# Performance work log

Measured on AMD Instinct MI355X. Metric: run time of the kernel, lower is better.

The kernel has to match this reference:

```python
import jax, jax.numpy as jnp
import numpy as np


def setup_inputs() -> dict:
    key = jax.random.key(0)
    ks = jax.random.split(key, 8)
    B, N, K, C_in, M, C_add, C_out = 2, 40000, 16, 64, 16, 3, 128
    in_features = (C_in + C_add) * M  # 1072
    input_features = jax.random.normal(ks[0], (B, N, C_in), dtype=jnp.float32)
    neighbor_inds = jax.random.randint(ks[1], (B, N, K), 0, N, dtype=jnp.int64)
    inverse_neighbors = jax.random.randint(ks[2], (B, N * K), 0, N * K, dtype=jnp.int64)
    inverse_k = jax.random.randint(ks[3], (B, N * K), 0, K, dtype=jnp.int64)
    inverse_idx = jax.random.randint(ks[4], (B, N * K), 0, N, dtype=jnp.int64)
    weightnet = jax.random.normal(ks[5], (B, N, K, M), dtype=jnp.float32)
    additional_features = jax.random.normal(ks[6], (B, N, K, C_add), dtype=jnp.float32)
    bound = 1.0 / np.sqrt(in_features)
    kw, kb = jax.random.split(ks[7])
    linear_weight = jax.random.uniform(kw, (C_out, in_features), dtype=jnp.float32, minval=-bound, maxval=bound)
    linear_bias = jax.random.uniform(kb, (C_out,), dtype=jnp.float32, minval=-bound, maxval=bound)
    return {
        "input_features": input_features,
        "neighbor_inds": neighbor_inds,
        "inverse_neighbors": inverse_neighbors,
        "inverse_k": inverse_k,
        "inverse_idx": inverse_idx,
        "weightnet": weightnet,
        "additional_features": additional_features,
        "linear_weight": linear_weight,
        "linear_bias": linear_bias,
    }


def reference(input_features, neighbor_inds, inverse_neighbors, inverse_k, inverse_idx,
              weightnet, additional_features, linear_weight, linear_bias):
    # inverse_* tensors are only used by the custom CUDA backward; unused here.
    B, N, K = neighbor_inds.shape
    # gather neighbor features: [B, N, K, C_in]
    gathered = jnp.take_along_axis(input_features[:, :, None, :],
                                   neighbor_inds[..., None], axis=1)
    # concat extra per-neighbor features -> [B, N, K, C]
    feats = jnp.concatenate([gathered, additional_features], axis=-1)
    # PConv: [B,N,C,K] @ [B,N,K,M] -> [B,N,C,M] -> flatten to [B,N,C*M]
    pconv = jnp.einsum('bnkc,bnkm->bncm', feats, weightnet)
    pconv = pconv.reshape(B, N, -1)
    # fused linear
    out = jnp.einsum('bnf,of->bno', pconv, linear_weight) + linear_bias
    return out
```

## Files before the change

### kernel.cpp

```cpp
#include <hip/hip_runtime.h>
#include <stdint.h>

typedef unsigned short u16;
typedef short short8 __attribute__((ext_vector_type(8)));
typedef float floatx4 __attribute__((ext_vector_type(4)));

#define NPERB   40000
#define NPTS    80000
#define KNBR    16
#define CIN     64
#define MDIM    16
#define CADD    3
#define CF      (CIN + CADD)
#define COUT    128
#define KF      1072
#define KP      1088
#define NKT     34
#define PTSB    16
#define SLAB    65
#define GR      128
#define PPB     8

__device__ __forceinline__ u16 f2bf(float f) {
    union { float f; unsigned int u; } v; v.f = f;
    unsigned int u = v.u;
    return (u16)((u + 0x7FFFu + ((u >> 16) & 1u)) >> 16);
}
__device__ __forceinline__ short8 pack8(floatx4 x, floatx4 y) {
    union { short8 v; u16 a[8]; } u;
    u.a[0] = f2bf(x[0]); u.a[1] = f2bf(x[1]); u.a[2] = f2bf(x[2]); u.a[3] = f2bf(x[3]);
    u.a[4] = f2bf(y[0]); u.a[5] = f2bf(y[1]); u.a[6] = f2bf(y[2]); u.a[7] = f2bf(y[3]);
    return u.v;
}
__device__ __forceinline__ unsigned swz(unsigned chunk) {
    return chunk ^ ((chunk >> 3) & 7u);
}
__device__ __forceinline__ void gload_lds16(const void* g, void* l) {
    __builtin_amdgcn_global_load_lds(
        (const __attribute__((address_space(1))) void*)g,
        (__attribute__((address_space(3))) void*)l, 16, 0, 0);
}

__global__ void prep_lw_kernel(const float* __restrict__ lw, u16* __restrict__ lwp) {
    int i = blockIdx.x * 256 + threadIdx.x;
    if (i >= COUT * KP) return;
    int o = i / KP, f = i - o * KP;
    lwp[i] = (f < KF) ? f2bf(lw[(size_t)o * KF + f]) : (u16)0;
}

__device__ __forceinline__ void emit_point(
    int lane, float av, const float (&fv)[KNBR], const float* wl,
    u16* __restrict__ dst)
{
    const int em = lane & 15, ec = lane >> 4;
    float ev = 0.f;
#pragma unroll
    for (int k = 0; k < KNBR; k++)
        ev += __shfl(av, k * CADD + ec) * wl[k * MDIM + em];
    if (ec == 3) ev = 0.f;
    dst[1024 + lane] = f2bf(ev);

    floatx4 a0 = 0, a1 = 0, a2 = 0, a3 = 0;
#pragma unroll
    for (int k = 0; k < KNBR; k++) {
        const floatx4* w4 = (const floatx4*)(wl + k * MDIM);
        const float fvk = fv[k];
        a0 += fvk * w4[0]; a1 += fvk * w4[1];
        a2 += fvk * w4[2]; a3 += fvk * w4[3];
    }
    *(short8*)(dst + lane * 16)     = pack8(a0, a1);
    *(short8*)(dst + lane * 16 + 8) = pack8(a2, a3);
}

__global__ __launch_bounds__(256) void pconv_kernel(
    const float* __restrict__ inp,
    const int*   __restrict__ nbr,
    const float* __restrict__ wn,
    const float* __restrict__ addl,
    u16* __restrict__ pc)
{
    __shared__ __align__(16) float Wns[PPB * KNBR * MDIM];

    const int wave = threadIdx.x >> 6;
    const int lane = threadIdx.x & 63;
    const int pbase = blockIdx.x * PPB;
    const float* inpb = inp + ((pbase >= NPERB) ? (size_t)NPERB * CIN : 0);

    const int pr0 = wave * 2;
    const int p0  = __builtin_amdgcn_readfirstlane(pbase + pr0);
    const int p1  = p0 + 1;

    float* wl0 = Wns + pr0 * (KNBR * MDIM);
    float* wl1 = wl0 + KNBR * MDIM;
    gload_lds16(wn + (size_t)p0 * (KNBR * MDIM) + lane * 4, wl0);
    gload_lds16(wn + (size_t)p1 * (KNBR * MDIM) + lane * 4, wl1);

    float av0 = (lane < KNBR * CADD) ? addl[(size_t)p0 * (KNBR * CADD) + lane] : 0.f;
    float av1 = (lane < KNBR * CADD) ? addl[(size_t)p1 * (KNBR * CADD) + lane] : 0.f;

    const int* nb0 = nbr + (size_t)p0 * KNBR;
    const int* nb1 = nbr + (size_t)p1 * KNBR;
    int idx0[KNBR], idx1[KNBR];
#pragma unroll
    for (int k = 0; k < KNBR; k++) idx0[k] = nb0[k];
#pragma unroll
    for (int k = 0; k < KNBR; k++) idx1[k] = nb1[k];

    float fv0[KNBR], fv1[KNBR];
#pragma unroll
    for (int k = 0; k < KNBR; k++) fv0[k] = inpb[(size_t)idx0[k] * CIN + lane];
#pragma unroll
    for (int k = 0; k < KNBR; k++) fv1[k] = inpb[(size_t)idx1[k] * CIN + lane];

    asm volatile("s_waitcnt vmcnt(0)" ::: "memory");
    __builtin_amdgcn_sched_barrier(0);

    emit_point(lane, av0, fv0, wl0, pc + (size_t)p0 * KP);
    emit_point(lane, av1, fv1, wl1, pc + (size_t)p1 * KP);
}

__global__ __launch_bounds__(256, 2) void gemm_kernel(
    const u16* __restrict__ pc,
    const u16* __restrict__ lwp,
    const float* __restrict__ bias,
    float* __restrict__ out)
{
    __shared__ __align__(16) u16 As[4][4][1024];

    const int wave = threadIdx.x >> 6;
    const int lane = threadIdx.x & 63;
    const int r16 = lane & 15, quad = lane >> 4;
    const int row0 = blockIdx.x * GR + wave * 32;

    const u16* aS0 = pc + (size_t)(row0 + r16) * KP + quad * 8;
    const u16* aS1 = aS0 + (size_t)16 * KP;
    u16* aD = &As[wave][0][0];

    const u16* bB = lwp + (size_t)r16 * KP + quad * 8;

    float bv[8];
#pragma unroll
    for (int n = 0; n < 8; n++) bv[n] = bias[n * 16 + r16];
    __builtin_amdgcn_sched_barrier(0);

    floatx4 acc0[8], acc1[8];
#pragma unroll
    for (int n = 0; n < 8; n++) { acc0[n] = 0; acc1[n] = 0; }

    short8 Bq[3][8];

#define STAGE(s) { \
    gload_lds16(aS0 + (s) * 32, aD + ((s) & 3) * 1024); \
    gload_lds16(aS1 + (s) * 32, aD + ((s) & 3) * 1024 + 512); }

#define LOADB(s) { \
    _Pragma("unroll") \
    for (int n = 0; n < 8; n++) \
        Bq[(s) % 3][n] = *(const short8*)(bB + (size_t)n * 16 * KP + (s) * 32); }

    STAGE(0); STAGE(1); STAGE(2);
    __builtin_amdgcn_sched_barrier(0);
    LOADB(0);
    __builtin_amdgcn_sched_barrier(0);
    LOADB(1);
    __builtin_amdgcn_sched_barrier(0);

#define STEP(kt, N) { \
    if ((kt) + 3 < NKT) STAGE((kt) + 3); \
    if ((kt) + 2 < NKT) LOADB((kt) + 2); \
    __builtin_amdgcn_sched_barrier(0); \
    asm volatile("s_waitcnt vmcnt(" #N ")"); \
    __builtin_amdgcn_sched_barrier(0); \
    short8 A0 = *(const short8*)(aD + ((kt) & 3) * 1024 + lane * 8); \
    short8 A1 = *(const short8*)(aD + ((kt) & 3) * 1024 + 512 + lane * 8); \
    asm volatile("s_waitcnt lgkmcnt(0)"); \
    __builtin_amdgcn_sched_barrier(0); \
    _Pragma("unroll") \
    for (int n = 0; n < 8; n++) { \
        acc0[n] = __builtin_amdgcn_mfma_f32_16x16x32_bf16(A0, Bq[(kt) % 3][n], acc0[n], 0, 0, 0); \
        acc1[n] = __builtin_amdgcn_mfma_f32_16x16x32_bf16(A1, Bq[(kt) % 3][n], acc1[n], 0, 0, 0); \
    } }

    STEP(0, 18)  STEP(1, 20)  STEP(2, 20)  STEP(3, 20)  STEP(4, 20)
    STEP(5, 20)  STEP(6, 20)  STEP(7, 20)  STEP(8, 20)  STEP(9, 20)
    STEP(10, 20) STEP(11, 20) STEP(12, 20) STEP(13, 20) STEP(14, 20)
    STEP(15, 20) STEP(16, 20) STEP(17, 20) STEP(18, 20) STEP(19, 20)
    STEP(20, 20) STEP(21, 20) STEP(22, 20) STEP(23, 20) STEP(24, 20)
    STEP(25, 20) STEP(26, 20) STEP(27, 20) STEP(28, 20) STEP(29, 20)
    STEP(30, 20) STEP(31, 18) STEP(32, 8)  STEP(33, 0)

#undef STEP
#undef LOADB
#undef STAGE

#pragma unroll
    for (int n = 0; n < 8; n++) {
#pragma unroll
        for (int r = 0; r < 4; r++) {
            size_t row = (size_t)(row0 + quad * 4 + r) * COUT;
            out[row + n * 16 + r16] = acc0[n][r] + bv[n];
            row = (size_t)(row0 + 16 + quad * 4 + r) * COUT;
            out[row + n * 16 + r16] = acc1[n][r] + bv[n];
        }
    }
}

__device__ __forceinline__ void compute_point(
    int pr, int lane, float av, const float (&fv)[KNBR],
    const float* wl, u16* Apc)
{
    const int em = lane & 15, ec = lane >> 4;
    float ev = 0.f;
#pragma unroll
    for (int k = 0; k < KNBR; k++)
        ev += __shfl(av, k * CADD + ec) * wl[k * MDIM + em];
    if (ec == 3) ev = 0.f;
    {
        unsigned kt   = 32 + (lane >> 5);
        unsigned quad = (lane >> 3) & 3;
        unsigned ch   = kt * SLAB + (unsigned)pr * 4 + quad;
        Apc[swz(ch) * 8 + (lane & 7)] = f2bf(ev);
    }
    floatx4 a0 = 0, a1 = 0, a2 = 0, a3 = 0;
#pragma unroll
    for (int k = 0; k < KNBR; k++) {
        const floatx4* w4 = (const floatx4*)(wl + k * MDIM);
        const float fvk = fv[k];
        a0 += fvk * w4[0]; a1 += fvk * w4[1];
        a2 += fvk * w4[2]; a3 += fvk * w4[3];
    }
    {
        unsigned kt = lane >> 1, qb = (lane & 1) * 2;
        unsigned ch = kt * SLAB + (unsigned)pr * 4 + qb;
        *(short8*)&Apc[swz(ch) * 8]     = pack8(a0, a1);
        *(short8*)&Apc[swz(ch + 1) * 8] = pack8(a2, a3);
    }
}

__global__ __launch_bounds__(512, 6) void fused_kernel(
    const float* __restrict__ inp, const int* __restrict__ nbr,
    const float* __restrict__ wn, const float* __restrict__ addl,
    const u16* __restrict__ lwp, const float* __restrict__ bias,
    float* __restrict__ out)
{
    __shared__ __align__(16) u16   Apc[(NKT * SLAB + 8) * 8];
    __shared__ __align__(16) float Wns[PTSB * KNBR * MDIM];

    const int wave = threadIdx.x >> 6;
    const int lane = threadIdx.x & 63;
    const int pbase = blockIdx.x * PTSB;
    const float* inpb = inp + ((pbase >= NPERB) ? (size_t)NPERB * CIN : 0);

    const int pr0 = wave * 2;
    const int p0  = __builtin_amdgcn_readfirstlane(pbase + pr0);
    const int p1  = p0 + 1;

    float* wl0 = Wns + pr0 * (KNBR * MDIM);
    float* wl1 = wl0 + KNBR * MDIM;
    gload_lds16(wn + (size_t)p0 * (KNBR * MDIM) + lane * 4, wl0);
    gload_lds16(wn + (size_t)p1 * (KNBR * MDIM) + lane * 4, wl1);

    float av0 = (lane < KNBR * CADD) ? addl[(size_t)p0 * (KNBR * CADD) + lane] : 0.f;
    float av1 = (lane < KNBR * CADD) ? addl[(size_t)p1 * (KNBR * CADD) + lane] : 0.f;

    const int* nb0 = nbr + (size_t)p0 * KNBR;
    const int* nb1 = nbr + (size_t)p1 * KNBR;
    int idx0[KNBR], idx1[KNBR];
#pragma unroll
    for (int k = 0; k < KNBR; k++) idx0[k] = nb0[k];
#pragma unroll
    for (int k = 0; k < KNBR; k++) idx1[k] = nb1[k];

    float fv0[KNBR], fv1[KNBR];
#pragma unroll
    for (int k = 0; k < KNBR; k++) fv0[k] = inpb[(size_t)idx0[k] * CIN + lane];
#pragma unroll
    for (int k = 0; k < KNBR; k++) fv1[k] = inpb[(size_t)idx1[k] * CIN + lane];

    asm volatile("s_waitcnt vmcnt(0)" ::: "memory");
    __builtin_amdgcn_sched_barrier(0);

    compute_point(pr0,     lane, av0, fv0, wl0, Apc);
    compute_point(pr0 + 1, lane, av1, fv1, wl1, Apc);

    const int r16 = lane & 15, quad = lane >> 4;
    const int c0 = wave * 16;
    const u16* Bp = lwp + (size_t)(c0 + r16) * KP + quad * 8;
    const unsigned abase = (unsigned)r16 * 4 + quad;
    const float bv = bias[c0 + r16];

    __syncthreads();

    floatx4 acc = 0;
#pragma unroll 2
    for (int kt = 0; kt < NKT; kt++) {
        short8 A = *(const short8*)&Apc[swz((unsigned)kt * SLAB + abase) * 8];
        short8 B = *(const short8*)(Bp + kt * 32);
        acc = __builtin_amdgcn_mfma_f32_16x16x32_bf16(A, B, acc, 0, 0, 0);
    }

#pragma unroll
    for (int r = 0; r < 4; r++) {
        const size_t row = (size_t)(pbase + quad * 4 + r) * COUT;
        out[row + c0 + r16] = acc[r] + bv;
    }
}

__global__ __launch_bounds__(256) void fused_fallback_kernel(
    const float* __restrict__ inp, const int* __restrict__ nbr,
    const float* __restrict__ wn, const float* __restrict__ addl,
    const float* __restrict__ lw, const float* __restrict__ bias,
    float* __restrict__ out)
{
    const int p = blockIdx.x;
    const int b = p / NPERB;
    const int tid = threadIdx.x;
    __shared__ float sf[KNBR * CF];
    __shared__ float sw[KNBR * MDIM];
    __shared__ float sp[KF];

    sw[tid] = wn[(size_t)p * (KNBR * MDIM) + tid];
    for (int i = tid; i < KNBR * CIN; i += 256) {
        int k = i >> 6, c = i & 63;
        int idx = nbr[(size_t)p * KNBR + k];
        sf[k * CF + c] = inp[((size_t)b * NPERB + idx) * CIN + c];
    }
    if (tid < KNBR * CADD) {
        int k = tid / CADD, c = tid - k * CADD;
        sf[k * CF + CIN + c] = addl[(size_t)p * (KNBR * CADD) + tid];
    }
    __syncthreads();
    for (int f = tid; f < KF; f += 256) {
        int c = f >> 4, m = f & 15;
        float s = 0;
#pragma unroll
        for (int k = 0; k < KNBR; k++) s += sf[k * CF + c] * sw[k * MDIM + m];
        sp[f] = s;
    }
    __syncthreads();
    const int o = tid >> 1, h = tid & 1;
    float s = 0;
    for (int f = h * (KF / 2); f < (h + 1) * (KF / 2); f++)
        s += sp[f] * lw[(size_t)o * KF + f];
    s += __shfl_xor(s, 1);
    if (h == 0) out[(size_t)p * COUT + o] = s + bias[o];
}

extern "C" void kernel_launch(void* const* d_in, const int* in_sizes, int n_in,
                              void* d_out, int out_size, void* d_ws, size_t ws_size,
                              hipStream_t stream) {
    const float* inp  = (const float*)d_in[0];
    const int*   nbr  = (const int*)d_in[1];
    const float* wn   = (const float*)d_in[5];
    const float* addl = (const float*)d_in[6];
    const float* lw   = (const float*)d_in[7];
    const float* bias = (const float*)d_in[8];
    float* out = (float*)d_out;

    const size_t lw_bytes = (size_t)COUT * KP * sizeof(u16);
    const size_t pc_bytes = (size_t)NPTS * KP * sizeof(u16);

    if (ws_size >= lw_bytes + pc_bytes) {
        u16* lwp = (u16*)d_ws;
        u16* pcw = lwp + (size_t)COUT * KP;
        prep_lw_kernel<<<(COUT * KP + 255) / 256, 256, 0, stream>>>(lw, lwp);
        pconv_kernel<<<NPTS / PPB, 256, 0, stream>>>(inp, nbr, wn, addl, pcw);
        gemm_kernel<<<NPTS / GR, 256, 0, stream>>>(pcw, lwp, bias, out);
    } else if (ws_size >= lw_bytes) {
        u16* lwp = (u16*)d_ws;
        prep_lw_kernel<<<(COUT * KP + 255) / 256, 256, 0, stream>>>(lw, lwp);
        fused_kernel<<<NPTS / PTSB, 512, 0, stream>>>(inp, nbr, wn, addl, lwp, bias, out);
    } else {
        fused_fallback_kernel<<<NPTS, 256, 0, stream>>>(inp, nbr, wn, addl, lw, bias, out);
    }
}
```

Before: 340.9 us.

## Split GEMM output columns across wave pairs with swizzled LDS A staging

The GEMM kernel now gives each block 64 rows instead of 128. Waves are paired so that each wave computes 32 rows by 64 output columns rather than 32 by 128. This halves per-wave B registers and accumulators and doubles the grid size, which is meant to raise occupancy and parallelism. The A tile staged in LDS now uses an XOR swizzle to avoid bank conflicts on reads, and the wait counts and load order are adjusted to match. In exchange, the pconv A data is loaded twice per block (once by each wave of a pair), raising global and L2 traffic for A.

```diff
diff --git a/kernel.cpp b/kernel.cpp
--- a/kernel.cpp
+++ b/kernel.cpp
@@ -18,7 +18,7 @@
 #define NKT     34
 #define PTSB    16
 #define SLAB    65
-#define GR      128
+#define GRB     64
 #define PPB     8
 
 __device__ __forceinline__ u16 f2bf(float f) {
@@ -119,88 +119,102 @@
     emit_point(lane, av1, fv1, wl1, pc + (size_t)p1 * KP);
 }
 
-__global__ __launch_bounds__(256, 2) void gemm_kernel(
+__global__ __launch_bounds__(256) void gemm_kernel(
     const u16* __restrict__ pc,
     const u16* __restrict__ lwp,
     const float* __restrict__ bias,
     float* __restrict__ out)
 {
-    __shared__ __align__(16) u16 As[4][4][1024];
+    __shared__ __align__(16) u16 As[4 * 4 * 1024];
 
     const int wave = threadIdx.x >> 6;
     const int lane = threadIdx.x & 63;
     const int r16 = lane & 15, quad = lane >> 4;
-    const int row0 = blockIdx.x * GR + wave * 32;
-
-    const u16* aS0 = pc + (size_t)(row0 + r16) * KP + quad * 8;
-    const u16* aS1 = aS0 + (size_t)16 * KP;
-    u16* aD = &As[wave][0][0];
-
-    const u16* bB = lwp + (size_t)r16 * KP + quad * 8;
-
-    float bv[8];
-#pragma unroll
-    for (int n = 0; n < 8; n++) bv[n] = bias[n * 16 + r16];
-    __builtin_amdgcn_sched_barrier(0);
-
-    floatx4 acc0[8], acc1[8];
-#pragma unroll
-    for (int n = 0; n < 8; n++) { acc0[n] = 0; acc1[n] = 0; }
-
-    short8 Bq[3][8];
+    const int rh = wave >> 1, ch = wave & 1;
+    const int row0 = blockIdx.x * GRB + rh * 32;
+    const int cb   = ch * 64;
+
+    const int srow = lane >> 2;
+    const int sq   = (lane & 3) ^ ((lane >> 3) & 3);
+    const u16* aS0 = pc + (size_t)(row0 + srow) * KP + sq * 8;
+    const u16* aS1 = pc + (size_t)(row0 + 16 + srow) * KP + sq * 8;
+    u16* aD = &As[wave * 4096];
+
+    const unsigned cA0 = (((unsigned)r16 << 2) | ((unsigned)quad ^ ((r16 >> 1) & 3))) << 3;
+
+    const u16* bB0 = lwp + (size_t)(cb + r16) * KP + quad * 8;
+    const u16* bB1 = bB0 + (size_t)16 * KP;
+    const u16* bB2 = bB0 + (size_t)32 * KP;
+    const u16* bB3 = bB0 + (size_t)48 * KP;
+
+    float bv[4];
+#pragma unroll
+    for (int n = 0; n < 4; n++) bv[n] = bias[cb + n * 16 + r16];
+    __builtin_amdgcn_sched_barrier(0);
+
+    floatx4 acc0[4], acc1[4];
+#pragma unroll
+    for (int n = 0; n < 4; n++) { acc0[n] = 0; acc1[n] = 0; }
+
+    short8 Bq[3][4];
 
 #define STAGE(s) { \
     gload_lds16(aS0 + (s) * 32, aD + ((s) & 3) * 1024); \
     gload_lds16(aS1 + (s) * 32, aD + ((s) & 3) * 1024 + 512); }
 
-#define LOADB(s) { \
-    _Pragma("unroll") \
-    for (int n = 0; n < 8; n++) \
-        Bq[(s) % 3][n] = *(const short8*)(bB + (size_t)n * 16 * KP + (s) * 32); }
-
-    STAGE(0); STAGE(1); STAGE(2);
-    __builtin_amdgcn_sched_barrier(0);
-    LOADB(0);
-    __builtin_amdgcn_sched_barrier(0);
-    LOADB(1);
+#define LOADB(t) { \
+    Bq[(t) % 3][0] = *(const short8*)(bB0 + (t) * 32); \
+    Bq[(t) % 3][1] = *(const short8*)(bB1 + (t) * 32); \
+    Bq[(t) % 3][2] = *(const short8*)(bB2 + (t) * 32); \
+    Bq[(t) % 3][3] = *(const short8*)(bB3 + (t) * 32); }
+
+    STAGE(0) STAGE(1) STAGE(2)
+    __builtin_amdgcn_sched_barrier(0);
+    LOADB(0)
+    __builtin_amdgcn_sched_barrier(0);
+    LOADB(1)
     __builtin_amdgcn_sched_barrier(0);
 
 #define STEP(kt, N) { \
-    if ((kt) + 3 < NKT) STAGE((kt) + 3); \
-    if ((kt) + 2 < NKT) LOADB((kt) + 2); \
+    if ((kt) + 2 < NKT) { LOADB((kt) + 2) __builtin_amdgcn_sched_barrier(0); } \
+    if ((kt) + 3 < NKT) { STAGE((kt) + 3) __builtin_amdgcn_sched_barrier(0); } \
+    asm volatile("s_waitcnt vmcnt(" #N ")" ::: "memory"); \
     __builtin_amdgcn_sched_barrier(0); \
-    asm volatile("s_waitcnt vmcnt(" #N ")"); \
-    __builtin_amdgcn_sched_barrier(0); \
-    short8 A0 = *(const short8*)(aD + ((kt) & 3) * 1024 + lane * 8); \
-    short8 A1 = *(const short8*)(aD + ((kt) & 3) * 1024 + 512 + lane * 8); \
-    asm volatile("s_waitcnt lgkmcnt(0)"); \
+    short8 A0 = *(const short8*)(aD + ((kt) & 3) * 1024 + cA0); \
+    short8 A1 = *(const short8*)(aD + ((kt) & 3) * 1024 + cA0 + 512); \
+    asm volatile("s_waitcnt lgkmcnt(0)" ::: "memory"); \
     __builtin_amdgcn_sched_barrier(0); \
     _Pragma("unroll") \
-    for (int n = 0; n < 8; n++) { \
+    for (int n = 0; n < 4; n++) { \
         acc0[n] = __builtin_amdgcn_mfma_f32_16x16x32_bf16(A0, Bq[(kt) % 3][n], acc0[n], 0, 0, 0); \
         acc1[n] = __builtin_amdgcn_mfma_f32_16x16x32_bf16(A1, Bq[(kt) % 3][n], acc1[n], 0, 0, 0); \
     } }
 
-    STEP(0, 18)  STEP(1, 20)  STEP(2, 20)  STEP(3, 20)  STEP(4, 20)
-    STEP(5, 20)  STEP(6, 20)  STEP(7, 20)  STEP(8, 20)  STEP(9, 20)
-    STEP(10, 20) STEP(11, 20) STEP(12, 20) STEP(13, 20) STEP(14, 20)
-    STEP(15, 20) STEP(16, 20) STEP(17, 20) STEP(18, 20) STEP(19, 20)
-    STEP(20, 20) STEP(21, 20) STEP(22, 20) STEP(23, 20) STEP(24, 20)
-    STEP(25, 20) STEP(26, 20) STEP(27, 20) STEP(28, 20) STEP(29, 20)
-    STEP(30, 20) STEP(31, 18) STEP(32, 8)  STEP(33, 0)
+    STEP(0, 10)  STEP(1, 12)  STEP(2, 14)  STEP(3, 14)  STEP(4, 14)
+    STEP(5, 14)  STEP(6, 14)  STEP(7, 14)  STEP(8, 14)  STEP(9, 14)
+    STEP(10, 14) STEP(11, 14) STEP(12, 14) STEP(13, 14) STEP(14, 14)
+    STEP(15, 14) STEP(16, 14) STEP(17, 14) STEP(18, 14) STEP(19, 14)
+    STEP(20, 14) STEP(21, 14) STEP(22, 14) STEP(23, 14) STEP(24, 14)
+    STEP(25, 14) STEP(26, 14) STEP(27, 14) STEP(28, 14) STEP(29, 14)
+    STEP(30, 14) STEP(31, 12) STEP(32, 6)  STEP(33, 0)
 
 #undef STEP
 #undef LOADB
 #undef STAGE
 
 #pragma unroll
-    for (int n = 0; n < 8; n++) {
-#pragma unroll
-        for (int r = 0; r < 4; r++) {
-            size_t row = (size_t)(row0 + quad * 4 + r) * COUT;
-            out[row + n * 16 + r16] = acc0[n][r] + bv[n];
-            row = (size_t)(row0 + 16 + quad * 4 + r) * COUT;
-            out[row + n * 16 + r16] = acc1[n][r] + bv[n];
+    for (int r = 0; r < 4; r++) {
+        {
+            const size_t row = (size_t)(row0 + quad * 4 + r) * COUT;
+#pragma unroll
+            for (int n = 0; n < 4; n++)
+                out[row + cb + n * 16 + r16] = acc0[n][r] + bv[n];
+        }
+        {
+            const size_t row = (size_t)(row0 + 16 + quad * 4 + r) * COUT;
+#pragma unroll
+            for (int n = 0; n < 4; n++)
+                out[row + cb + n * 16 + r16] = acc1[n][r] + bv[n];
         }
     }
 }
@@ -365,7 +379,7 @@
         u16* pcw = lwp + (size_t)COUT * KP;
         prep_lw_kernel<<<(COUT * KP + 255) / 256, 256, 0, stream>>>(lw, lwp);
         pconv_kernel<<<NPTS / PPB, 256, 0, stream>>>(inp, nbr, wn, addl, pcw);
-        gemm_kernel<<<NPTS / GR, 256, 0, stream>>>(pcw, lwp, bias, out);
+        gemm_kernel<<<NPTS / GRB, 256, 0, stream>>>(pcw, lwp, bias, out);
     } else if (ws_size >= lw_bytes) {
         u16* lwp = (u16*)d_ws;
         prep_lw_kernel<<<(COUT * KP + 255) / 256, 256, 0, stream>>>(lw, lwp);
```

Result: no change. 335.3 us (-1.7%).
